# Kernel tuning notes

Hardware: AMD Instinct MI355X
Metric: run time of the kernel (lower is better)

## Reference

```python
import jax, jax.numpy as jnp
import numpy as np

D_MODEL = 1024
NUM_HEADS = 16
HEAD_DIM = D_MODEL // NUM_HEADS


def setup_inputs() -> dict:
    key = jax.random.key(0)
    ks = jax.random.split(key, 10)
    B, SQ, SK = 2, 2048, 2048
    scale = 1.0 / np.sqrt(D_MODEL)
    inp = {
        "x1": jax.random.normal(ks[0], (B, SQ, D_MODEL), jnp.float32),
        "x2": jax.random.normal(ks[1], (B, SK, D_MODEL), jnp.float32),
        "Wq": jax.random.normal(ks[2], (D_MODEL, D_MODEL), jnp.float32) * scale,
        "bq": jnp.zeros((D_MODEL,), jnp.float32),
        "Wk": jax.random.normal(ks[3], (D_MODEL, D_MODEL), jnp.float32) * scale,
        "bk": jnp.zeros((D_MODEL,), jnp.float32),
        "Wv": jax.random.normal(ks[4], (D_MODEL, D_MODEL), jnp.float32) * scale,
        "bv": jnp.zeros((D_MODEL,), jnp.float32),
        "Wo": jax.random.normal(ks[5], (D_MODEL, D_MODEL), jnp.float32) * scale,
        "bo": jnp.zeros((D_MODEL,), jnp.float32),
    }
    return inp


def reference(x1, x2, Wq, bq, Wk, bk, Wv, bv, Wo, bo):
    B, SQ, _ = x1.shape
    SK = x2.shape[1]
    # projections, then split into heads: [B, H, S, Dh]
    def split_heads(t, S):
        return t.reshape(B, S, NUM_HEADS, HEAD_DIM).transpose(0, 2, 1, 3)
    Q = split_heads(x1 @ Wq + bq, SQ)
    K = split_heads(x2 @ Wk + bk, SK)
    V = split_heads(x2 @ Wv + bv, SK)
    # note: original scales by 1/head_dim**0.5
    scores = jnp.einsum("bhqd,bhkd->bhqk", Q, K) / jnp.sqrt(
        jnp.asarray(HEAD_DIM, Q.dtype))
    attn = jax.nn.softmax(scores, axis=-1)
    ctx = jnp.einsum("bhqk,bhkd->bhqd", attn, V)
    ctx = ctx.transpose(0, 2, 1, 3).reshape(B, SQ, D_MODEL)
    return ctx @ Wo + bo
```

## Files before the change

### kernel.cpp

```cpp
#include <hip/hip_runtime.h>
#include <stdint.h>


typedef unsigned short u16b;
typedef __attribute__((ext_vector_type(4))) short short4v;
typedef __attribute__((ext_vector_type(8))) short short8v;
typedef __attribute__((ext_vector_type(4))) float float4v;
typedef __attribute__((ext_vector_type(16))) float float16v;
typedef __attribute__((ext_vector_type(2))) unsigned int uint2v;

#if __has_builtin(__builtin_amdgcn_exp2f)
__device__ __forceinline__ float exp2_fast(float x){ return __builtin_amdgcn_exp2f(x); }
#else
__device__ __forceinline__ float exp2_fast(float x){ return exp2f(x); }
#endif

__device__ __forceinline__ u16b f2bf(float f) {
  union { float f; unsigned int i; } v; v.f = f;
  return (u16b)((v.i + 0x7fffu + ((v.i >> 16) & 1u)) >> 16);
}
__device__ __forceinline__ void gl_lds16(const u16b* g, u16b* l) {
  __builtin_amdgcn_global_load_lds(
      (const __attribute__((address_space(1))) void*)g,
      (__attribute__((address_space(3))) void*)l, 16, 0, 0);
}

#define FENCE_BARRIER() do { asm volatile("" ::: "memory"); \
  __builtin_amdgcn_s_barrier(); asm volatile("" ::: "memory"); } while(0)
#define LGKM0() do { asm volatile("s_waitcnt lgkmcnt(0)" ::: "memory"); \
  __builtin_amdgcn_sched_barrier(0); } while(0)
#define VMCNT(n) do { asm volatile("s_waitcnt vmcnt(" #n ")" ::: "memory"); \
  __builtin_amdgcn_sched_barrier(0); } while(0)

__global__ __launch_bounds__(256) void prep(
    const float* __restrict__ x1, const float* __restrict__ x2,
    const float* __restrict__ W0, const float* __restrict__ W1,
    const float* __restrict__ W2, const float* __restrict__ W3,
    u16b* __restrict__ x1b, u16b* __restrict__ x2b, u16b* __restrict__ WT) {
  const int tid = threadIdx.x;
  const int mode = blockIdx.y;
  if (mode < 2) {
    const float* src = mode ? x2 : x1;
    u16b* dst = mode ? x2b : x1b;
    const int n4 = 1024*1024;
    int i = blockIdx.x * 256 + tid;
    const int stride = gridDim.x * 256;
    for (; i < n4; i += stride) {
      float4v v = ((const float4v*)src)[i];
      short4v o;
      o[0]=(short)f2bf(v[0]); o[1]=(short)f2bf(v[1]);
      o[2]=(short)f2bf(v[2]); o[3]=(short)f2bf(v[3]);
      ((short4v*)dst)[i] = o;
    }
  } else {
    __shared__ u16b tile[32][33];
    const int z = mode - 2;
    const float* src = (z==0) ? W0 : (z==1) ? W1 : (z==2) ? W2 : W3;
    u16b* dst = WT + (size_t)z * (1024*1024);
    const int x = tid & 31, y = tid >> 5;
    const int bx = (blockIdx.x & 31) * 32, by = (blockIdx.x >> 5) * 32;
#pragma unroll
    for (int j=0;j<4;++j)
      tile[y*4+j][x] = f2bf(src[(size_t)(by + y*4+j)*1024 + bx + x]);
    __syncthreads();
#pragma unroll
    for (int j=0;j<4;++j)
      dst[(size_t)(bx + y*4+j)*1024 + by + x] = tile[x][y*4+j];
  }
}

template<bool BIAS_ROW>
__device__ __forceinline__ void gemm256_core(
    u16b* __restrict__ As, u16b* __restrict__ Bs,
    const u16b* __restrict__ A, const u16b* __restrict__ Bt,
    const float* __restrict__ bias, u16b* __restrict__ C,
    int N, int K, int bm, int bn, float oscale) {
  constexpr int ASTR = 256*64, BSTR = 256*64;
  const int tid = threadIdx.x;
  const int lane = tid & 63, wave = tid >> 6;
  const int wr = wave >> 2, wc = wave & 3;
  const int l15 = lane & 15, l4 = lane >> 4;

  auto stage_half = [&](const u16b* __restrict__ G, int row0, int k0,
                        u16b* __restrict__ Lbase) {
#pragma unroll
    for (int j=0;j<2;++j) {
      int idx = j*512 + tid;
      int row = idx >> 3, seg = idx & 7;
      int segg = seg ^ (row & 7);
      gl_lds16(&G[(size_t)(row0+row)*K + k0 + segg*8], &Lbase[idx*8]);
    }
  };

  float4v acc[2][2][4][2];
#pragma unroll
  for (int qm=0;qm<2;++qm)
#pragma unroll
  for (int qn=0;qn<2;++qn)
#pragma unroll
  for (int m=0;m<4;++m)
#pragma unroll
  for (int n=0;n<2;++n) acc[qm][qn][m][n] = (float4v){0.f,0.f,0.f,0.f};

  const int NK = K >> 6;
  stage_half(A,  bm+0,   0,  As + 0);
  stage_half(Bt, bn+0,   0,  Bs + 0);
  stage_half(A,  bm+128, 0,  As + 128*64);
  stage_half(Bt, bn+128, 0,  Bs + 128*64);
  stage_half(A,  bm+0,   64, As + ASTR);
  stage_half(Bt, bn+0,   64, Bs + BSTR);
  VMCNT(4);
  FENCE_BARRIER();

  int cur = 0;
  for (int t = 0; t < NK; ++t) {
    u16b* Ac = As + cur*ASTR;  u16b* Bc = Bs + cur*BSTR;
    u16b* An = As + (cur^1)*ASTR;  u16b* Bn = Bs + (cur^1)*BSTR;
    const int k1 = (t+1) << 6, k2 = (t+2) << 6;
    short8v af[4][2], bf0[2][2], bf1[2][2];

#pragma unroll
    for (int m=0;m<4;++m)
#pragma unroll
      for (int ks=0;ks<2;++ks)
        af[m][ks] = *(const short8v*)&Ac[(0*128 + wr*64 + m*16 + l15)*64
                                         + (((ks*4+l4) ^ (l15&7))*8)];
#pragma unroll
    for (int n=0;n<2;++n)
#pragma unroll
      for (int ks=0;ks<2;++ks)
        bf0[n][ks] = *(const short8v*)&Bc[(0*128 + wc*32 + n*16 + l15)*64
                                          + (((ks*4+l4) ^ (l15&7))*8)];
    if (t+1 < NK) stage_half(A, bm+128, k1, An + 128*64);
    FENCE_BARRIER();
    LGKM0();
    __builtin_amdgcn_s_setprio(1);
#pragma unroll
    for (int m=0;m<4;++m)
#pragma unroll
      for (int n=0;n<2;++n)
#pragma unroll
        for (int ks=0;ks<2;++ks)
          acc[0][0][m][n] = __builtin_amdgcn_mfma_f32_16x16x32_bf16(
              af[m][ks], bf0[n][ks], acc[0][0][m][n], 0, 0, 0);
    __builtin_amdgcn_s_setprio(0);
    FENCE_BARRIER();

#pragma unroll
    for (int n=0;n<2;++n)
#pragma unroll
      for (int ks=0;ks<2;++ks)
        bf1[n][ks] = *(const short8v*)&Bc[(1*128 + wc*32 + n*16 + l15)*64
                                          + (((ks*4+l4) ^ (l15&7))*8)];
    if (t+1 < NK) stage_half(Bt, bn+128, k1, Bn + 128*64);
    FENCE_BARRIER();
    LGKM0();
    __builtin_amdgcn_s_setprio(1);
#pragma unroll
    for (int m=0;m<4;++m)
#pragma unroll
      for (int n=0;n<2;++n)
#pragma unroll
        for (int ks=0;ks<2;++ks)
          acc[0][1][m][n] = __builtin_amdgcn_mfma_f32_16x16x32_bf16(
              af[m][ks], bf1[n][ks], acc[0][1][m][n], 0, 0, 0);
    __builtin_amdgcn_s_setprio(0);
    FENCE_BARRIER();

#pragma unroll
    for (int m=0;m<4;++m)
#pragma unroll
      for (int ks=0;ks<2;++ks)
        af[m][ks] = *(const short8v*)&Ac[(1*128 + wr*64 + m*16 + l15)*64
                                         + (((ks*4+l4) ^ (l15&7))*8)];
    if (t+2 < NK) stage_half(A, bm+0, k2, Ac + 0);
    FENCE_BARRIER();
    LGKM0();
    __builtin_amdgcn_s_setprio(1);
#pragma unroll
    for (int m=0;m<4;++m)
#pragma unroll
      for (int n=0;n<2;++n)
#pragma unroll
        for (int ks=0;ks<2;++ks)
          acc[1][0][m][n] = __builtin_amdgcn_mfma_f32_16x16x32_bf16(
              af[m][ks], bf0[n][ks], acc[1][0][m][n], 0, 0, 0);
    __builtin_amdgcn_s_setprio(0);
    FENCE_BARRIER();

    if (t+2 < NK) stage_half(Bt, bn+0, k2, Bc + 0);
    FENCE_BARRIER();
    LGKM0();
    __builtin_amdgcn_s_setprio(1);
#pragma unroll
    for (int m=0;m<4;++m)
#pragma unroll
      for (int n=0;n<2;++n)
#pragma unroll
        for (int ks=0;ks<2;++ks)
          acc[1][1][m][n] = __builtin_amdgcn_mfma_f32_16x16x32_bf16(
              af[m][ks], bf1[n][ks], acc[1][1][m][n], 0, 0, 0);
    __builtin_amdgcn_s_setprio(0);
    if (t == NK-2) { VMCNT(0); }
    else          { VMCNT(4); }
    FENCE_BARRIER();
    cur ^= 1;
  }

#pragma unroll
  for (int qm=0;qm<2;++qm)
#pragma unroll
  for (int qn=0;qn<2;++qn)
#pragma unroll
  for (int n=0;n<2;++n) {
    int col = bn + qn*128 + wc*32 + n*16 + l15;
    float bbc = BIAS_ROW ? 0.f : bias[col];
#pragma unroll
    for (int m=0;m<4;++m) {
      int row0 = bm + qm*128 + wr*64 + m*16 + l4*4;
#pragma unroll
      for (int r=0;r<4;++r) {
        float bb = BIAS_ROW ? bias[row0+r] : bbc;
        float v = (acc[qm][qn][m][n][r] + bb) * oscale;
        C[(size_t)(row0+r)*N + col] = f2bf(v);
      }
    }
  }
}

__global__ __launch_bounds__(512, 2) void gemm_qkv256(
    const u16b* __restrict__ x1b, const u16b* __restrict__ x2b,
    const u16b* __restrict__ WT, const float* __restrict__ bq,
    const float* __restrict__ bk, const float* __restrict__ bv,
    u16b* __restrict__ QKV) {
  __shared__ __align__(16) u16b As[2*256*64];
  __shared__ __align__(16) u16b Bs[2*256*64];
  const int f = blockIdx.x;
  const int z = f >> 6;
  const int u = f & 63;
  const int w = ((u & 7) << 3) | (u >> 3);
  const size_t Mi = 1024*1024;
  const float QSCALE = 0.125f * 1.4426950408889634f;
  if (z == 2) {
    int bm = (w >> 4) * 256;
    int bn = (w & 15) * 256;
    gemm256_core<true>(As, Bs, WT + 2*Mi, x2b, bv, QKV + 8*Mi,
                       4096, 1024, bm, bn, 1.0f);
  } else {
    int bm = (w >> 2) * 256;
    int bn = (w & 3) * 256;
    gemm256_core<false>(As, Bs, z ? x2b : x1b, WT + (size_t)z*Mi,
                        z ? bk : bq, QKV + (size_t)z*4*Mi,
                        1024, 1024, bm, bn, z ? 1.0f : QSCALE);
  }
}

template<int BN, bool OUT_F32, bool BIAS_ROW>
__device__ __forceinline__ void gemm_core(
    u16b* __restrict__ As, u16b* __restrict__ Bs,
    const u16b* __restrict__ A, const u16b* __restrict__ Bt,
    const float* __restrict__ bias, void* __restrict__ Cv,
    int N, int K, int bm, int bn, float oscale) {
  constexpr int NT = BN / 32;
  constexpr int ASTRIDE = 128*64;
  constexpr int BSTRIDE = BN*64;
  const int tid = threadIdx.x;
  const int lane = tid & 63, wave = tid >> 6;
  const int wm = wave >> 1, wn = wave & 1;
  const int l15 = lane & 15, l4 = lane >> 4;
  float4v acc[4][NT];
#pragma unroll
  for (int i=0;i<4;++i)
#pragma unroll
    for (int j=0;j<NT;++j) acc[i][j] = (float4v){0.f,0.f,0.f,0.f};

  auto stage = [&](int buf, int k0) {
#pragma unroll
    for (int j=0;j<4;++j) {
      int idx = j*256 + tid;
      int row = idx >> 3, seg = idx & 7;
      int segg = seg ^ (row & 7);
      gl_lds16(&A[(size_t)(bm+row)*K + k0 + segg*8], &As[buf*ASTRIDE + idx*8]);
    }
#pragma unroll
    for (int j=0;j<BN/32;++j) {
      int idx = j*256 + tid;
      int row = idx >> 3, seg = idx & 7;
      int segg = seg ^ (row & 7);
      gl_lds16(&Bt[(size_t)(bn+row)*K + k0 + segg*8], &Bs[buf*BSTRIDE + idx*8]);
    }
  };

  const int NK = K >> 6;
  stage(0, 0);
  __syncthreads();
  for (int kt = 0; kt < NK; ++kt) {
    const int cur = kt & 1;
    if (kt + 1 < NK) stage(cur ^ 1, (kt + 1) << 6);
    const u16b* Asb = As + cur*ASTRIDE;
    const u16b* Bsb = Bs + cur*BSTRIDE;
#pragma unroll
    for (int ks=0; ks<2; ++ks) {
      short8v af[4], bf[NT];
      const int cs = ((ks*4 + l4) ^ (l15 & 7)) * 8;
#pragma unroll
      for (int mt=0;mt<4;++mt)
        af[mt] = *(const short8v*)&Asb[(wm*64+mt*16+l15)*64 + cs];
#pragma unroll
      for (int nt=0;nt<NT;++nt)
        bf[nt] = *(const short8v*)&Bsb[(wn*(BN/2)+nt*16+l15)*64 + cs];
#pragma unroll
      for (int mt=0;mt<4;++mt)
#pragma unroll
        for (int nt=0;nt<NT;++nt)
          acc[mt][nt] = __builtin_amdgcn_mfma_f32_16x16x32_bf16(af[mt], bf[nt], acc[mt][nt], 0, 0, 0);
    }
    __syncthreads();
  }

#pragma unroll
  for (int nt=0;nt<NT;++nt) {
    int col = bn + wn*(BN/2) + nt*16 + l15;
    float bbc = BIAS_ROW ? 0.f : bias[col];
#pragma unroll
    for (int mt=0;mt<4;++mt) {
      int row0 = bm + wm*64 + mt*16 + l4*4;
#pragma unroll
      for (int r=0;r<4;++r) {
        float bb = BIAS_ROW ? bias[row0+r] : bbc;
        float v = (acc[mt][nt][r] + bb) * oscale;
        if (OUT_F32) ((float*)Cv)[(size_t)(row0+r)*N + col] = v;
        else         ((u16b*)Cv)[(size_t)(row0+r)*N + col] = f2bf(v);
      }
    }
  }
}

__global__ __launch_bounds__(256) void gemm_out(
    const u16b* __restrict__ A, const u16b* __restrict__ Bt,
    const float* __restrict__ bias, float* __restrict__ C) {
  __shared__ __align__(16) u16b As[2*128*64];
  __shared__ __align__(16) u16b Bs[2*64*64];
  const int f = blockIdx.x;
  const int xcd = f & 7, s = f >> 3;
  const int bm = (xcd*4 + (s >> 4)) * 128;
  const int bn = (s & 15) * 64;
  gemm_core<64,true,false>(As, Bs, A, Bt, bias, C, 1024, 1024, bm, bn, 1.0f);
}

__device__ __forceinline__ void attn_load(
    const u16b* __restrict__ Kgb, const u16b* __restrict__ Vtb,
    int kvoff, int tid, short8v kreg[4], short8v vreg[4]) {
#pragma unroll
  for (int j=0; j<4; ++j) {
    int idx = j*256 + tid;
    int rowk = idx >> 3, segk = idx & 7;
    kreg[j] = *(const short8v*)&Kgb[(size_t)(kvoff+rowk)*1024 + ((segk ^ (rowk & 7))*8)];
    int rowv = idx & 63, segv = idx >> 6;
    vreg[j] = *(const short8v*)&Vtb[(size_t)rowv*4096 + kvoff + segv*8];
  }
}

__global__ __launch_bounds__(256, 2) void attn_q128(
    const u16b* __restrict__ Q, const u16b* __restrict__ Kg,
    const u16b* __restrict__ Vt, u16b* __restrict__ O) {
  __shared__ __align__(16) u16b Ks[2][128*64];
  __shared__ __align__(16) u16b Vs[2][64*132];
  const int tid = threadIdx.x;
  const int lane = tid & 63, wave = tid >> 6;
  const int l31 = lane & 31, hi = lane >> 5;
  const int bh = blockIdx.x;
  const int b = bh >> 4, h = bh & 15;
  const int q0 = blockIdx.y * 128;
  const size_t seqbase = (size_t)b * 2048;
  const int colh = h * 64;
  const u16b* Kgb = Kg + seqbase*1024 + colh;
  const u16b* Vtb = Vt + (size_t)(h*64)*4096 + (size_t)b*2048;

  short8v kreg[4], vreg[4];
  attn_load(Kgb, Vtb, 0, tid, kreg, vreg);

  short8v qf[4];
  {
    size_t qrow = seqbase + q0 + wave*32 + l31;
#pragma unroll
    for (int ks=0; ks<4; ++ks)
      qf[ks] = *(const short8v*)&Q[qrow*1024 + colh + ks*16 + hi*8];
  }

  float16v oacc[2];
#pragma unroll
  for (int nb=0; nb<2; ++nb)
#pragma unroll
    for (int r=0; r<16; ++r) oacc[nb][r] = 0.f;
  float lsum = 0.f;

  {
    u16b* Kw = Ks[0]; u16b* Vw = Vs[0];
#pragma unroll
    for (int j=0; j<4; ++j) {
      int idx = j*256 + tid;
      *(short8v*)&Kw[idx*8] = kreg[j];
      int rowv = idx & 63, segv = idx >> 6;
      union { short8v s; uint2v u[2]; } tv; tv.s = vreg[j];
      *(uint2v*)&Vw[rowv*132 + segv*8]     = tv.u[0];
      *(uint2v*)&Vw[rowv*132 + segv*8 + 4] = tv.u[1];
    }
  }

  for (int kt = 0; kt < 16; ++kt) {
    __syncthreads();
    if (kt < 15)
      attn_load(Kgb, Vtb, (kt+1)*128, tid, kreg, vreg);
    const u16b* Kb_ = Ks[kt & 1];
    const u16b* Vb_ = Vs[kt & 1];

    float16v sacc[4];
#pragma unroll
    for (int kb=0; kb<4; ++kb)
#pragma unroll
      for (int r=0; r<16; ++r) sacc[kb][r] = 0.f;
    __builtin_amdgcn_s_setprio(1);
#pragma unroll
    for (int kb=0; kb<4; ++kb)
#pragma unroll
      for (int ks=0; ks<4; ++ks) {
        int row = kb*32 + l31;
        short8v kf = *(const short8v*)&Kb_[row*64 + (((ks*2+hi) ^ (row & 7))*8)];
        sacc[kb] = __builtin_amdgcn_mfma_f32_32x32x16_bf16(kf, qf[ks], sacc[kb], 0, 0, 0);
      }
    __builtin_amdgcn_s_setprio(0);

#pragma unroll
    for (int kb=0; kb<4; ++kb) {
      float e[16];
#pragma unroll
      for (int r=0; r<16; ++r) e[r] = exp2_fast(sacc[kb][r]);
#pragma unroll
      for (int r=0; r<16; ++r) lsum += e[r];
      unsigned int d[8];
#pragma unroll
      for (int i=0; i<8; ++i)
        d[i] = __builtin_amdgcn_perm(__float_as_uint(e[2*i+1]),
                                     __float_as_uint(e[2*i]), 0x07060302u);
      union { unsigned int u[4]; short8v s; } pa0, pa1;
      pa0.u[0]=d[0]; pa0.u[1]=d[1]; pa0.u[2]=d[2]; pa0.u[3]=d[3];
      pa1.u[0]=d[4]; pa1.u[1]=d[5]; pa1.u[2]=d[6]; pa1.u[3]=d[7];
      __builtin_amdgcn_s_setprio(1);
#pragma unroll
      for (int nb=0; nb<2; ++nb) {
        int row = nb*32 + l31;
        const u16b* vb = &Vb_[row*132 + kb*32 + hi*4];
        union { short4v h[2]; short8v s; } v0, v1;
        v0.h[0] = *(const short4v*)(vb);
        v0.h[1] = *(const short4v*)(vb + 8);
        v1.h[0] = *(const short4v*)(vb + 16);
        v1.h[1] = *(const short4v*)(vb + 24);
        oacc[nb] = __builtin_amdgcn_mfma_f32_32x32x16_bf16(pa0.s, v0.s, oacc[nb], 0, 0, 0);
        oacc[nb] = __builtin_amdgcn_mfma_f32_32x32x16_bf16(pa1.s, v1.s, oacc[nb], 0, 0, 0);
      }
      __builtin_amdgcn_s_setprio(0);
    }

    if (kt < 15) {
      u16b* Kw = Ks[(kt+1) & 1]; u16b* Vw = Vs[(kt+1) & 1];
#pragma unroll
      for (int j=0; j<4; ++j) {
        int idx = j*256 + tid;
        *(short8v*)&Kw[idx*8] = kreg[j];
        int rowv = idx & 63, segv = idx >> 6;
        union { short8v s; uint2v u[2]; } tv; tv.s = vreg[j];
        *(uint2v*)&Vw[rowv*132 + segv*8]     = tv.u[0];
        *(uint2v*)&Vw[rowv*132 + segv*8 + 4] = tv.u[1];
      }
    }
  }

  float ltot = lsum + __shfl_xor(lsum, 32, 64);
#pragma unroll
  for (int r=0; r<16; ++r) {
    int qloc = (r & 3) + 8*(r >> 2) + 4*hi;
    float lv = __shfl(ltot, qloc, 64);
    float inv = 1.0f / lv;
    size_t row = seqbase + q0 + wave*32 + qloc;
    O[row*1024 + colh +      l31] = f2bf(oacc[0][r] * inv);
    O[row*1024 + colh + 32 + l31] = f2bf(oacc[1][r] * inv);
  }
}

extern "C" void kernel_launch(void* const* d_in, const int* in_sizes, int n_in,
                              void* d_out, int out_size, void* d_ws, size_t ws_size,
                              hipStream_t stream) {
  const float* x1 = (const float*)d_in[0];
  const float* x2 = (const float*)d_in[1];
  const float* Wq = (const float*)d_in[2];
  const float* bq = (const float*)d_in[3];
  const float* Wk = (const float*)d_in[4];
  const float* bk = (const float*)d_in[5];
  const float* Wv = (const float*)d_in[6];
  const float* bv = (const float*)d_in[7];
  const float* Wo = (const float*)d_in[8];
  const float* bo = (const float*)d_in[9];
  (void)in_sizes; (void)n_in; (void)out_size; (void)ws_size;

  u16b* ws = (u16b*)d_ws;
  const size_t Mi = 1024*1024;
  u16b* WT  = ws;
  u16b* WoT = ws + 3*Mi;
  u16b* x1b = ws + 4*Mi;
  u16b* x2b = ws + 8*Mi;
  u16b* QKV = ws + 12*Mi;
  u16b* Qb  = QKV;
  u16b* Kb  = QKV + 4*Mi;
  u16b* Vtb = QKV + 8*Mi;
  u16b* Cx  = x1b;

  prep<<<dim3(1024,6), 256, 0, stream>>>(x1, x2, Wq, Wk, Wv, Wo, x1b, x2b, WT);

  gemm_qkv256<<<dim3(192), 512, 0, stream>>>(x1b, x2b, WT, bq, bk, bv, QKV);

  attn_q128<<<dim3(32,16), 256, 0, stream>>>(Qb, Kb, Vtb, Cx);

  gemm_out<<<dim3(512), 256, 0, stream>>>(Cx, WoT, bo, (float*)d_out);
}
```

Before: 197.4 us.

## Double query rows per attention block and widen output GEMM tiles

```diff
diff --git a/kernel.cpp b/kernel.cpp
--- a/kernel.cpp
+++ b/kernel.cpp
@@ -340,12 +340,12 @@
     const u16b* __restrict__ A, const u16b* __restrict__ Bt,
     const float* __restrict__ bias, float* __restrict__ C) {
   __shared__ __align__(16) u16b As[2*128*64];
-  __shared__ __align__(16) u16b Bs[2*64*64];
+  __shared__ __align__(16) u16b Bs[2*128*64];
   const int f = blockIdx.x;
   const int xcd = f & 7, s = f >> 3;
-  const int bm = (xcd*4 + (s >> 4)) * 128;
-  const int bn = (s & 15) * 64;
-  gemm_core<64,true,false>(As, Bs, A, Bt, bias, C, 1024, 1024, bm, bn, 1.0f);
+  const int bm = (xcd*4 + (s >> 3)) * 128;
+  const int bn = (s & 7) * 128;
+  gemm_core<128,true,false>(As, Bs, A, Bt, bias, C, 1024, 1024, bm, bn, 1.0f);
 }
 
 __device__ __forceinline__ void attn_load(
@@ -361,7 +361,21 @@
   }
 }
 
-__global__ __launch_bounds__(256, 2) void attn_q128(
+__device__ __forceinline__ void attn_stage(
+    u16b* __restrict__ Kw, u16b* __restrict__ Vw,
+    int tid, const short8v kreg[4], const short8v vreg[4]) {
+#pragma unroll
+  for (int j=0; j<4; ++j) {
+    int idx = j*256 + tid;
+    *(short8v*)&Kw[idx*8] = kreg[j];
+    int rowv = idx & 63, segv = idx >> 6;
+    union { short8v s; uint2v u[2]; } tv; tv.s = vreg[j];
+    *(uint2v*)&Vw[rowv*132 + segv*8]     = tv.u[0];
+    *(uint2v*)&Vw[rowv*132 + segv*8 + 4] = tv.u[1];
+  }
+}
+
+__global__ __launch_bounds__(256, 1) void attn_q256(
     const u16b* __restrict__ Q, const u16b* __restrict__ Kg,
     const u16b* __restrict__ Vt, u16b* __restrict__ O) {
   __shared__ __align__(16) u16b Ks[2][128*64];
@@ -371,7 +385,7 @@
   const int l31 = lane & 31, hi = lane >> 5;
   const int bh = blockIdx.x;
   const int b = bh >> 4, h = bh & 15;
-  const int q0 = blockIdx.y * 128;
+  const int q0 = blockIdx.y * 256;
   const size_t seqbase = (size_t)b * 2048;
   const int colh = h * 64;
   const u16b* Kgb = Kg + seqbase*1024 + colh;
@@ -380,33 +394,27 @@
   short8v kreg[4], vreg[4];
   attn_load(Kgb, Vtb, 0, tid, kreg, vreg);
 
-  short8v qf[4];
-  {
-    size_t qrow = seqbase + q0 + wave*32 + l31;
+  short8v qf[2][4];
+#pragma unroll
+  for (int qb=0; qb<2; ++qb) {
+    size_t qrow = seqbase + q0 + wave*64 + qb*32 + l31;
 #pragma unroll
     for (int ks=0; ks<4; ++ks)
-      qf[ks] = *(const short8v*)&Q[qrow*1024 + colh + ks*16 + hi*8];
-  }
-
-  float16v oacc[2];
-#pragma unroll
-  for (int nb=0; nb<2; ++nb)
-#pragma unroll
-    for (int r=0; r<16; ++r) oacc[nb][r] = 0.f;
-  float lsum = 0.f;
-
-  {
-    u16b* Kw = Ks[0]; u16b* Vw = Vs[0];
-#pragma unroll
-    for (int j=0; j<4; ++j) {
-      int idx = j*256 + tid;
-      *(short8v*)&Kw[idx*8] = kreg[j];
-      int rowv = idx & 63, segv = idx >> 6;
-      union { short8v s; uint2v u[2]; } tv; tv.s = vreg[j];
-      *(uint2v*)&Vw[rowv*132 + segv*8]     = tv.u[0];
-      *(uint2v*)&Vw[rowv*132 + segv*8 + 4] = tv.u[1];
-    }
-  }
+      qf[qb][ks] = *(const short8v*)&Q[qrow*1024 + colh + ks*16 + hi*8];
+  }
+
+  float16v oacc[2][2][2];
+#pragma unroll
+  for (int qb=0; qb<2; ++qb)
+#pragma unroll
+    for (int nb=0; nb<2; ++nb)
+#pragma unroll
+      for (int p=0; p<2; ++p)
+#pragma unroll
+        for (int r=0; r<16; ++r) oacc[qb][nb][p][r] = 0.f;
+  float lsum[2] = {0.f, 0.f};
+
+  attn_stage(Ks[0], Vs[0], tid, kreg, vreg);
 
   for (int kt = 0; kt < 16; ++kt) {
     __syncthreads();
@@ -415,37 +423,46 @@
     const u16b* Kb_ = Ks[kt & 1];
     const u16b* Vb_ = Vs[kt & 1];
 
-    float16v sacc[4];
-#pragma unroll
-    for (int kb=0; kb<4; ++kb)
-#pragma unroll
-      for (int r=0; r<16; ++r) sacc[kb][r] = 0.f;
-    __builtin_amdgcn_s_setprio(1);
-#pragma unroll
-    for (int kb=0; kb<4; ++kb)
+#pragma unroll
+    for (int kb=0; kb<4; ++kb) {
+      short8v kf[4];
 #pragma unroll
       for (int ks=0; ks<4; ++ks) {
         int row = kb*32 + l31;
-        short8v kf = *(const short8v*)&Kb_[row*64 + (((ks*2+hi) ^ (row & 7))*8)];
-        sacc[kb] = __builtin_amdgcn_mfma_f32_32x32x16_bf16(kf, qf[ks], sacc[kb], 0, 0, 0);
+        kf[ks] = *(const short8v*)&Kb_[row*64 + (((ks*2+hi) ^ (row & 7))*8)];
       }
-    __builtin_amdgcn_s_setprio(0);
-
-#pragma unroll
-    for (int kb=0; kb<4; ++kb) {
-      float e[16];
-#pragma unroll
-      for (int r=0; r<16; ++r) e[r] = exp2_fast(sacc[kb][r]);
-#pragma unroll
-      for (int r=0; r<16; ++r) lsum += e[r];
-      unsigned int d[8];
-#pragma unroll
-      for (int i=0; i<8; ++i)
-        d[i] = __builtin_amdgcn_perm(__float_as_uint(e[2*i+1]),
-                                     __float_as_uint(e[2*i]), 0x07060302u);
-      union { unsigned int u[4]; short8v s; } pa0, pa1;
-      pa0.u[0]=d[0]; pa0.u[1]=d[1]; pa0.u[2]=d[2]; pa0.u[3]=d[3];
-      pa1.u[0]=d[4]; pa1.u[1]=d[5]; pa1.u[2]=d[6]; pa1.u[3]=d[7];
+      float16v sacc[2];
+#pragma unroll
+      for (int qb=0; qb<2; ++qb)
+#pragma unroll
+        for (int r=0; r<16; ++r) sacc[qb][r] = 0.f;
+      __builtin_amdgcn_s_setprio(1);
+#pragma unroll
+      for (int ks=0; ks<4; ++ks) {
+        sacc[0] = __builtin_amdgcn_mfma_f32_32x32x16_bf16(kf[ks], qf[0][ks], sacc[0], 0, 0, 0);
+        sacc[1] = __builtin_amdgcn_mfma_f32_32x32x16_bf16(kf[ks], qf[1][ks], sacc[1], 0, 0, 0);
+      }
+      __builtin_amdgcn_s_setprio(0);
+
+      short8v pa0[2], pa1[2];
+#pragma unroll
+      for (int qb=0; qb<2; ++qb) {
+        float e[16];
+#pragma unroll
+        for (int r=0; r<16; ++r) e[r] = exp2_fast(sacc[qb][r]);
+#pragma unroll
+        for (int r=0; r<16; ++r) lsum[qb] += e[r];
+        unsigned int d[8];
+#pragma unroll
+        for (int i=0; i<8; ++i)
+          d[i] = __builtin_amdgcn_perm(__float_as_uint(e[2*i+1]),
+                                       __float_as_uint(e[2*i]), 0x07060302u);
+        union { unsigned int u[4]; short8v s; } a0, a1;
+        a0.u[0]=d[0]; a0.u[1]=d[1]; a0.u[2]=d[2]; a0.u[3]=d[3];
+        a1.u[0]=d[4]; a1.u[1]=d[5]; a1.u[2]=d[6]; a1.u[3]=d[7];
+        pa0[qb] = a0.s; pa1[qb] = a1.s;
+      }
+
       __builtin_amdgcn_s_setprio(1);
 #pragma unroll
       for (int nb=0; nb<2; ++nb) {
@@ -456,35 +473,30 @@
         v0.h[1] = *(const short4v*)(vb + 8);
         v1.h[0] = *(const short4v*)(vb + 16);
         v1.h[1] = *(const short4v*)(vb + 24);
-        oacc[nb] = __builtin_amdgcn_mfma_f32_32x32x16_bf16(pa0.s, v0.s, oacc[nb], 0, 0, 0);
-        oacc[nb] = __builtin_amdgcn_mfma_f32_32x32x16_bf16(pa1.s, v1.s, oacc[nb], 0, 0, 0);
+        oacc[0][nb][0] = __builtin_amdgcn_mfma_f32_32x32x16_bf16(pa0[0], v0.s, oacc[0][nb][0], 0, 0, 0);
+        oacc[0][nb][1] = __builtin_amdgcn_mfma_f32_32x32x16_bf16(pa1[0], v1.s, oacc[0][nb][1], 0, 0, 0);
+        oacc[1][nb][0] = __builtin_amdgcn_mfma_f32_32x32x16_bf16(pa0[1], v0.s, oacc[1][nb][0], 0, 0, 0);
+        oacc[1][nb][1] = __builtin_amdgcn_mfma_f32_32x32x16_bf16(pa1[1], v1.s, oacc[1][nb][1], 0, 0, 0);
       }
       __builtin_amdgcn_s_setprio(0);
     }
 
-    if (kt < 15) {
-      u16b* Kw = Ks[(kt+1) & 1]; u16b* Vw = Vs[(kt+1) & 1];
-#pragma unroll
-      for (int j=0; j<4; ++j) {
-        int idx = j*256 + tid;
-        *(short8v*)&Kw[idx*8] = kreg[j];
-        int rowv = idx & 63, segv = idx >> 6;
-        union { short8v s; uint2v u[2]; } tv; tv.s = vreg[j];
-        *(uint2v*)&Vw[rowv*132 + segv*8]     = tv.u[0];
-        *(uint2v*)&Vw[rowv*132 + segv*8 + 4] = tv.u[1];
-      }
-    }
-  }
-
-  float ltot = lsum + __shfl_xor(lsum, 32, 64);
-#pragma unroll
-  for (int r=0; r<16; ++r) {
-    int qloc = (r & 3) + 8*(r >> 2) + 4*hi;
-    float lv = __shfl(ltot, qloc, 64);
-    float inv = 1.0f / lv;
-    size_t row = seqbase + q0 + wave*32 + qloc;
-    O[row*1024 + colh +      l31] = f2bf(oacc[0][r] * inv);
-    O[row*1024 + colh + 32 + l31] = f2bf(oacc[1][r] * inv);
+    if (kt < 15)
+      attn_stage(Ks[(kt+1) & 1], Vs[(kt+1) & 1], tid, kreg, vreg);
+  }
+
+#pragma unroll
+  for (int qb=0; qb<2; ++qb) {
+    float ltot = lsum[qb] + __shfl_xor(lsum[qb], 32, 64);
+#pragma unroll
+    for (int r=0; r<16; ++r) {
+      int qloc = (r & 3) + 8*(r >> 2) + 4*hi;
+      float lv = __shfl(ltot, qloc, 64);
+      float inv = 1.0f / lv;
+      size_t row = seqbase + q0 + wave*64 + qb*32 + qloc;
+      O[row*1024 + colh +      l31] = f2bf((oacc[qb][0][0][r] + oacc[qb][0][1][r]) * inv);
+      O[row*1024 + colh + 32 + l31] = f2bf((oacc[qb][1][0][r] + oacc[qb][1][1][r]) * inv);
+    }
   }
 }
 
@@ -519,7 +531,7 @@
 
   gemm_qkv256<<<dim3(192), 512, 0, stream>>>(x1b, x2b, WT, bq, bk, bv, QKV);
 
-  attn_q128<<<dim3(32,16), 256, 0, stream>>>(Qb, Kb, Vtb, Cx);
-
-  gemm_out<<<dim3(512), 256, 0, stream>>>(Cx, WoT, bo, (float*)d_out);
-}
+  attn_q256<<<dim3(32,8), 256, 0, stream>>>(Qb, Kb, Vtb, Cx);
+
+  gemm_out<<<dim3(256), 256, 0, stream>>>(Cx, WoT, bo, (float*)d_out);
+}
```

Result: slower. 212.1 us (+7.4%).
